# Optimization experiments

Measured on AMD Instinct MI355X. Metric: run time of the kernel, lower is better.

Reference implementation:

```python
import jax, jax.numpy as jnp
import numpy as np

B, T, C = 2, 1024, 1024
H = 16
D = C // H          # 64 head_dim
NHH = 4             # hyper n_heads
NL = 2              # hyper n_layers
RANK = 8
SCALE = 16.0 / RANK # alpha / rank


def _rope(x, cos, sin):
    # x: (B,H,T,D); cos/sin: (1,1,T,D//2)
    xe, xo = x[..., ::2], x[..., 1::2]
    return jnp.stack((xe * cos - xo * sin, xe * sin + xo * cos), axis=-1).reshape(x.shape)


def _mha(x, w_in, b_in, w_out, b_out, mask):
    # torch nn.MultiheadAttention (batch_first) with additive causal mask
    b, t, d = x.shape
    dh = d // NHH
    qkv = x @ w_in.T + b_in
    q, k, v = jnp.split(qkv, 3, axis=-1)
    split = lambda z: z.reshape(b, t, NHH, dh).transpose(0, 2, 1, 3)
    q, k, v = split(q), split(k), split(v)
    s = jnp.einsum('bhqd,bhkd->bhqk', q, k) / jnp.sqrt(jnp.float32(dh)) + mask
    o = jnp.einsum('bhqk,bhkd->bhqd', jax.nn.softmax(s, axis=-1), v)
    o = o.transpose(0, 2, 1, 3).reshape(b, t, d)
    return o @ w_out.T + b_out


def _tiny_head(x_h, in_w, in_b, out_w, out_b, a_w, b_w, mask):
    # x_h: (B,T,D); per-layer params stacked on axis 0 (NL)
    out = x_h
    for l in range(NL):
        out = _mha(out, in_w[l], in_b[l], out_w[l], out_b[l], mask)
    ctx = out.mean(axis=1)                       # (B,D)
    A = (ctx @ a_w.T).reshape(-1, D, RANK)       # (B,D,R)
    Bm = (ctx @ b_w.T).reshape(-1, RANK, D)      # (B,R,D)
    return A, Bm


def reference(x, cos, sin, c_attn_w, c_attn_b, c_proj_w, c_proj_b,
              hyper_in_w, hyper_in_b, hyper_out_w, hyper_out_b, toA_w, toB_w):
    mask = jnp.where(jnp.tril(jnp.ones((T, T), bool)), 0.0, -jnp.inf).astype(x.dtype)
    qkv = x @ c_attn_w.T + c_attn_b
    q, k, v = jnp.split(qkv, 3, axis=-1)
    split = lambda z: z.reshape(B, T, H, D).transpose(0, 2, 1, 3)  # (B,H,T,D)
    q, k, v = split(q), split(k), split(v)
    q = _rope(q, cos, sin)
    k = _rope(k, cos, sin)
    x_heads = split(x)
    # vmap over the 16 main heads; each gets its own TinyHeadTransformer params
    A, Bm = jax.vmap(_tiny_head, in_axes=(1, 0, 0, 0, 0, 0, 0, None))(
        x_heads, hyper_in_w, hyper_in_b, hyper_out_w, hyper_out_b, toA_w, toB_w, mask)
    # A: (H,B,D,R), Bm: (H,B,R,D)
    delta_v = jnp.einsum('bhti,hbir,hbro->bhto', v, A, Bm)
    v = v + SCALE * delta_v
    s = jnp.einsum('bhqd,bhkd->bhqk', q, k) / jnp.sqrt(jnp.float32(D)) + mask
    y = jnp.einsum('bhqk,bhkd->bhqd', jax.nn.softmax(s, axis=-1), v)
    y = y.transpose(0, 2, 1, 3).reshape(B, T, C)
    return y @ c_proj_w.T + c_proj_b


def setup_inputs() -> dict:
    key = jax.random.key(0)
    ks = jax.random.split(key, 8)
    inv_freq = 1.0 / (10000.0 ** (jnp.arange(0, D, 2, dtype=jnp.float32) / D))
    ang = jnp.arange(T, dtype=jnp.float32)[:, None] * inv_freq[None, :]
    cos = jnp.cos(ang)[None, None]  # (1,1,T,D/2)
    sin = jnp.sin(ang)[None, None]
    g = lambda k, shape, sc: jax.random.normal(k, shape, jnp.float32) * sc
    return dict(
        x=g(ks[0], (B, T, C), 1.0),
        cos=cos, sin=sin,
        c_attn_w=g(ks[1], (3 * C, C), 0.02),
        c_attn_b=jnp.zeros((3 * C,), jnp.float32),
        c_proj_w=g(ks[2], (C, C), 0.02),
        c_proj_b=jnp.zeros((C,), jnp.float32),
        hyper_in_w=g(ks[3], (H, NL, 3 * D, D), 0.02),
        hyper_in_b=jnp.zeros((H, NL, 3 * D), jnp.float32),
        hyper_out_w=g(ks[4], (H, NL, D, D), 0.02),
        hyper_out_b=jnp.zeros((H, NL, D), jnp.float32),
        toA_w=g(ks[5], (H, D * RANK, D), 0.02),
        toB_w=g(ks[6], (H, RANK * D, D), 0.02),
    )
```

## Files before the change

### kernel.cpp

```cpp
#include <hip/hip_runtime.h>

typedef unsigned short u16;
typedef short v8s __attribute__((ext_vector_type(8)));
typedef short v4s16 __attribute__((ext_vector_type(4)));
typedef float v4f __attribute__((ext_vector_type(4)));

#if defined(__has_builtin)
#  if __has_builtin(__builtin_amdgcn_exp2f)
#    define EXP2F(x) __builtin_amdgcn_exp2f(x)
#  else
#    define EXP2F(x) exp2f(x)
#  endif
#else
#  define EXP2F(x) exp2f(x)
#endif

__device__ __forceinline__ float bf2f(u16 u){
  union { float f; unsigned int i; } c; c.i = ((unsigned int)u) << 16; return c.f;
}
__device__ __forceinline__ u16 f2bf(float f){
  union { float f; unsigned int i; } c; c.f = f;
  unsigned int r = c.i + 0x7FFFu + ((c.i >> 16) & 1u);
  return (u16)(r >> 16);
}
__device__ __forceinline__ unsigned int cvt_pk_bf16(float lo, float hi){
  unsigned int r;
  asm("v_cvt_pk_bf16_f32 %0, %1, %2" : "=v"(r) : "v"(lo), "v"(hi));
  return r;
}

struct CvtArgs {
  const float* s[13];
  u16* d[13];
  int n[13];
  int bstart[14];
};
__global__ __launch_bounds__(256) void cvt_all(CvtArgs a) {
  int j = 0;
  #pragma unroll
  for (int i = 1; i < 13; i++) if ((int)blockIdx.x >= a.bstart[i]) j = i;
  const int lb = blockIdx.x - a.bstart[j];
  const long base = (long)lb * 1024 + threadIdx.x * 4;
  if (base < a.n[j]) {
    const float4 f = *(const float4*)&a.s[j][base];
    v4s16 o;
    o.x = (short)f2bf(f.x); o.y = (short)f2bf(f.y);
    o.z = (short)f2bf(f.z); o.w = (short)f2bf(f.w);
    *(v4s16*)&a.d[j][base] = o;
  }
}

template<int BM, int BN, bool OUTF>
__global__ __launch_bounds__(256) void gemm_nt(
    const u16* __restrict__ A, long aBatch, int lda,
    const u16* __restrict__ W, long wBatch,
    const u16* __restrict__ bias, long bBatch,
    void* __restrict__ Cp, long cBatch, int ldc,
    int K)
{
  constexpr int BK = 64, LDT = BK + 8;
  constexpr int AC = BM / 32;
  constexpr int BC = BN / 32;
  A    += (long)blockIdx.z * aBatch;
  W    += (long)blockIdx.z * wBatch;
  bias += (long)blockIdx.z * bBatch;
  const int row0 = blockIdx.y * BM, col0 = blockIdx.x * BN;
  __shared__ __align__(16) u16 As[BM * LDT];
  __shared__ __align__(16) u16 Bs[BN * LDT];
  const int tid = threadIdx.x, wid = tid >> 6, lane = tid & 63;
  constexpr int FM = (BM/2)/16, FN = (BN/2)/16;
  const int wr = (wid >> 1) * (BM/2), wc = (wid & 1) * (BN/2);
  v4f acc[FM][FN] = {};
  const int lr = lane & 15, lk = (lane >> 4) * 8;

  v8s areg[AC], breg[BC];
  auto loadAB = [&](int k0) {
    #pragma unroll
    for (int i = 0; i < AC; i++) {
      const int c = tid + i*256, r = c >> 3, cc = (c & 7) * 8;
      areg[i] = *(const v8s*)&A[(long)(row0 + r)*lda + k0 + cc];
    }
    #pragma unroll
    for (int i = 0; i < BC; i++) {
      const int c = tid + i*256, r = c >> 3, cc = (c & 7) * 8;
      breg[i] = *(const v8s*)&W[(long)(col0 + r)*K + k0 + cc];
    }
  };
  auto writeAB = [&]() {
    #pragma unroll
    for (int i = 0; i < AC; i++) {
      const int c = tid + i*256, r = c >> 3, cc = (c & 7) * 8;
      *(v8s*)&As[r*LDT + cc] = areg[i];
    }
    #pragma unroll
    for (int i = 0; i < BC; i++) {
      const int c = tid + i*256, r = c >> 3, cc = (c & 7) * 8;
      *(v8s*)&Bs[r*LDT + cc] = breg[i];
    }
  };

  loadAB(0); writeAB();
  __syncthreads();
  for (int k0 = 0; k0 < K; k0 += BK) {
    if (k0 + BK < K) loadAB(k0 + BK);
    #pragma unroll
    for (int ks = 0; ks < BK; ks += 32) {
      v8s af[FM], bfv[FN];
      #pragma unroll
      for (int i = 0; i < FM; i++) af[i]  = *(const v8s*)&As[(wr + i*16 + lr)*LDT + ks + lk];
      #pragma unroll
      for (int j = 0; j < FN; j++) bfv[j] = *(const v8s*)&Bs[(wc + j*16 + lr)*LDT + ks + lk];
      #pragma unroll
      for (int i = 0; i < FM; i++)
        #pragma unroll
        for (int j = 0; j < FN; j++)
          acc[i][j] = __builtin_amdgcn_mfma_f32_16x16x32_bf16(af[i], bfv[j], acc[i][j], 0, 0, 0);
    }
    __syncthreads();
    if (k0 + BK < K) {
      writeAB();
      __syncthreads();
    }
  }
  const int lc = lane & 15, lq = (lane >> 4) * 4;
  u16*   Cb = (u16*)Cp   + (long)blockIdx.z * cBatch;
  float* Cf = (float*)Cp + (long)blockIdx.z * cBatch;
  #pragma unroll
  for (int i = 0; i < FM; i++)
    #pragma unroll
    for (int j = 0; j < FN; j++) {
      const int cidx = col0 + wc + j*16 + lc;
      const float bv = bf2f(bias[cidx]);
      #pragma unroll
      for (int q = 0; q < 4; q++) {
        const int r = row0 + wr + i*16 + lq + q;
        if (OUTF) Cf[(long)r*ldc + cidx] = acc[i][j][q] + bv;
        else      Cb[(long)r*ldc + cidx] = f2bf(acc[i][j][q] + bv);
      }
    }
}

__global__ __launch_bounds__(256) void rope_split_k(
    const u16* __restrict__ qkv, const u16* __restrict__ cosb, const u16* __restrict__ sinb,
    u16* __restrict__ qr, u16* __restrict__ kr, u16* __restrict__ vv)
{
  const int idx  = blockIdx.x * 4 + (threadIdx.x >> 6);
  const int lane = threadIdx.x & 63;
  const int t = idx & 1023;
  const int h = (idx >> 10) & 15;
  const int b = idx >> 14;
  const u16* base = qkv + ((long)(b*1024 + t))*3072 + h*64;
  const int i = lane >> 1;
  const float c = bf2f(cosb[t*32 + i]), s = bf2f(sinb[t*32 + i]);
  const long ro = (long)idx * 64 + lane;
  float xe = bf2f(base[2*i]), xo = bf2f(base[2*i + 1]);
  qr[ro] = f2bf((lane & 1) ? xe*s + xo*c : xe*c - xo*s);
  xe = bf2f(base[1024 + 2*i]); xo = bf2f(base[1024 + 2*i + 1]);
  kr[ro] = f2bf((lane & 1) ? xe*s + xo*c : xe*c - xo*s);
  vv[ro] = base[2048 + lane];
}

template<int D>
__global__ __launch_bounds__(512) void flash_mfma(
    const u16* __restrict__ qb, const u16* __restrict__ kb,
    const u16* __restrict__ vb, u16* __restrict__ ob,
    float scale, int n1, int n2,
    long q0, long q1, long q2, int qs,
    long k0, long k1, long k2, int ks,
    long v0, long v1, long v2, int vs,
    long o0, long o1, long o2, int os)
{
  constexpr int KBLK = 64;
  constexpr int KD2 = (D < 32) ? 32 : D;
  constexpr int LDK = KD2 + 8;
  constexpr int LDV = KBLK + 8;
  constexpr int KD  = KD2 / 32;
  constexpr int NSUB = D / 16;
  constexpr int KCH = KBLK * (KD2/8);
  constexpr int VCH = (D/8) * KBLK;
  __shared__ __align__(16) u16 Ks[2][KBLK * LDK];
  __shared__ __align__(16) u16 Vs[2][D * LDV];

  const int tid = threadIdx.x, wid = tid >> 6, lane = tid & 63;
  const int lr = lane & 15, lg = lane >> 4;
  const int prob = blockIdx.x;
  const int p2 = prob % n2, p1 = (prob / n2) % n1, p0 = prob / (n2 * n1);
  const u16* qp = qb + p0*q0 + p1*q1 + p2*q2;
  const u16* kp = kb + p0*k0 + p1*k1 + p2*k2;
  const u16* vp = vb + p0*v0 + p1*v1 + p2*v2;
  u16* op = ob + p0*o0 + p1*o1 + p2*o2;

  const int ta = blockIdx.y;
  const int tb = 15 - ta;
  const int wtile = (wid & 4) ? tb : ta;
  const int wq = wtile * 64 + (wid & 3) * 16;
  const float scale2 = scale * 1.44269504f;

  v8s qf[KD];
  #pragma unroll
  for (int kd = 0; kd < KD; kd++) {
    const int dof = kd*32 + lg*8;
    v8s val = {};
    if (dof < D) val = *(const v8s*)&qp[(long)(wq + lr)*qs + dof];
    qf[kd] = val;
  }

  v4f Of[NSUB] = {};
  float m2 = -1.0e30f, l = 0.f;

  const int kkey = tid / (KD2/8), kd8 = (tid % (KD2/8)) * 8;
  const int vkey = tid / (D/8),  vd8 = (tid % (D/8)) * 8;
  v8s kreg = {}, vreg = {};

  if (tid < KCH) { v8s t = {}; if (kd8 < D) t = *(const v8s*)&kp[(long)kkey*ks + kd8]; kreg = t; }
  if (tid < VCH) vreg = *(const v8s*)&vp[(long)vkey*vs + vd8];
  if (tid < KCH) *(v8s*)&Ks[0][kkey*LDK + kd8] = kreg;
  if (tid < VCH) {
    #pragma unroll
    for (int j = 0; j < 8; j++) Vs[0][(vd8+j)*LDV + vkey] = vreg[j];
  }
  __syncthreads();

  for (int c = 0; c <= tb; c++) {
    const int cur = c & 1, nxt = cur ^ 1;
    if (c < tb) {
      const int kc2 = (c + 1) * 64;
      if (tid < KCH) { v8s t = {}; if (kd8 < D) t = *(const v8s*)&kp[(long)(kc2+kkey)*ks + kd8]; kreg = t; }
      if (tid < VCH) vreg = *(const v8s*)&vp[(long)(kc2+vkey)*vs + vd8];
    }
    if (c <= wtile) {
      const int kc = c * 64;
      v4f sf[4];
      #pragma unroll
      for (int f = 0; f < 4; f++) {
        v4f s = {};
        #pragma unroll
        for (int kd = 0; kd < KD; kd++) {
          const v8s kf = *(const v8s*)&Ks[cur][(f*16 + lr)*LDK + kd*32 + lg*8];
          s = __builtin_amdgcn_mfma_f32_16x16x32_bf16(kf, qf[kd], s, 0, 0, 0);
        }
        sf[f] = s;
      }
      const int qg = wq + lr;
      if (kc + 63 > wq) {
        #pragma unroll
        for (int f = 0; f < 4; f++)
          #pragma unroll
          for (int r = 0; r < 4; r++)
            sf[f][r] = (kc + 16*f + 4*lg + r <= qg) ? sf[f][r] : -3.0e38f;
      }
      float mx0 = fmaxf(fmaxf(sf[0][0], sf[0][1]), fmaxf(sf[0][2], sf[0][3]));
      float mx1 = fmaxf(fmaxf(sf[1][0], sf[1][1]), fmaxf(sf[1][2], sf[1][3]));
      float mx2 = fmaxf(fmaxf(sf[2][0], sf[2][1]), fmaxf(sf[2][2], sf[2][3]));
      float mx3 = fmaxf(fmaxf(sf[3][0], sf[3][1]), fmaxf(sf[3][2], sf[3][3]));
      float mx = fmaxf(fmaxf(mx0, mx1), fmaxf(mx2, mx3));
      mx = fmaxf(mx, __shfl_xor(mx, 16));
      mx = fmaxf(mx, __shfl_xor(mx, 32));
      const float mn2 = fmaxf(m2, mx * scale2);
      const float al = EXP2F(m2 - mn2);
      m2 = mn2;
      float pv[4][4];
      #pragma unroll
      for (int f = 0; f < 4; f++)
        #pragma unroll
        for (int r = 0; r < 4; r++)
          pv[f][r] = EXP2F(__builtin_fmaf(sf[f][r], scale2, -mn2));
      float s0 = (pv[0][0]+pv[0][1]) + (pv[0][2]+pv[0][3]);
      float s1 = (pv[1][0]+pv[1][1]) + (pv[1][2]+pv[1][3]);
      float s2 = (pv[2][0]+pv[2][1]) + (pv[2][2]+pv[2][3]);
      float s3 = (pv[3][0]+pv[3][1]) + (pv[3][2]+pv[3][3]);
      float ps = (s0+s1) + (s2+s3);
      ps += __shfl_xor(ps, 16);
      ps += __shfl_xor(ps, 32);
      l = l * al + ps;
      #pragma unroll
      for (int sub = 0; sub < NSUB; sub++)
        #pragma unroll
        for (int r = 0; r < 4; r++) Of[sub][r] *= al;
      unsigned int pw[8];
      #pragma unroll
      for (int f = 0; f < 4; f++) {
        pw[2*f]   = cvt_pk_bf16(pv[f][0], pv[f][1]);
        pw[2*f+1] = cvt_pk_bf16(pv[f][2], pv[f][3]);
      }
      #pragma unroll
      for (int kb2 = 0; kb2 < 2; kb2++) {
        union { unsigned int w[4]; v8s v; } pb;
        pb.w[0] = pw[4*kb2];   pb.w[1] = pw[4*kb2+1];
        pb.w[2] = pw[4*kb2+2]; pb.w[3] = pw[4*kb2+3];
        #pragma unroll
        for (int sub = 0; sub < NSUB; sub++) {
          union { v4s16 h[2]; v8s v; } va;
          const int vbase = (sub*16 + lr)*LDV + kb2*32 + 4*lg;
          va.h[0] = *(const v4s16*)&Vs[cur][vbase];
          va.h[1] = *(const v4s16*)&Vs[cur][vbase + 16];
          Of[sub] = __builtin_amdgcn_mfma_f32_16x16x32_bf16(va.v, pb.v, Of[sub], 0, 0, 0);
        }
      }
    }
    if (c < tb) {
      if (tid < KCH) *(v8s*)&Ks[nxt][kkey*LDK + kd8] = kreg;
      if (tid < VCH) {
        #pragma unroll
        for (int j = 0; j < 8; j++) Vs[nxt][(vd8+j)*LDV + vkey] = vreg[j];
      }
    }
    __syncthreads();
  }
  const float rl = __builtin_amdgcn_rcpf(l);
  #pragma unroll
  for (int sub = 0; sub < NSUB; sub++) {
    unsigned int w0 = cvt_pk_bf16(Of[sub][0]*rl, Of[sub][1]*rl);
    unsigned int w1 = cvt_pk_bf16(Of[sub][2]*rl, Of[sub][3]*rl);
    unsigned int* dst = (unsigned int*)&op[(long)(wq + lr)*os + sub*16 + 4*lg];
    dst[0] = w0; dst[1] = w1;
  }
}

__global__ __launch_bounds__(256) void ctx_mean_k(const u16* __restrict__ tb, float* __restrict__ ctx)
{
  const int hb = blockIdx.x;
  const int h = hb >> 1, b = hb & 1;
  const int d = threadIdx.x & 63, chunk = threadIdx.x >> 6;
  const u16* p = tb + (long)h*2048*64 + (long)b*1024*64 + d;
  float s = 0.f;
  for (int t = chunk*256; t < (chunk+1)*256; t++) s += bf2f(p[(long)t*64]);
  __shared__ float red[4][64];
  red[chunk][d] = s;
  __syncthreads();
  if (threadIdx.x < 64) {
    const float tot = red[0][d] + red[1][d] + red[2][d] + red[3][d];
    ctx[hb*64 + d] = tot * (1.0f/1024.0f);
  }
}

__global__ __launch_bounds__(256) void ab_proj_k(const float* __restrict__ ctx,
    const u16* __restrict__ toA, const u16* __restrict__ toB,
    float* __restrict__ Am, float* __restrict__ Bm)
{
  const int hb = blockIdx.x; const int h = hb >> 1;
  const float* c = ctx + hb * 64;
  for (int n = threadIdx.x; n < 512; n += 256) {
    const u16* wa = toA + ((long)h*512 + n) * 64;
    const u16* wb = toB + ((long)h*512 + n) * 64;
    float sa = 0.f, sb = 0.f;
    for (int i = 0; i < 64; i++) { sa += c[i]*bf2f(wa[i]); sb += c[i]*bf2f(wb[i]); }
    Am[hb*512 + n] = sa;
    Bm[hb*512 + n] = sb;
  }
}

__global__ __launch_bounds__(256) void delta_v_k(
    u16* __restrict__ v, const float* __restrict__ Am, const float* __restrict__ Bm)
{
  const long idx = (long)blockIdx.x * blockDim.x + threadIdx.x;
  const int h = (int)((idx >> 10) & 15);
  const int b = (int)(idx >> 14);
  u16* row = v + idx * 64;
  const float* A = Am + (h*2 + b) * 512;
  const float* B = Bm + (h*2 + b) * 512;
  float tmp[8] = {};
  #pragma unroll 8
  for (int d = 0; d < 64; d++) {
    const float vd = bf2f(row[d]);
    #pragma unroll
    for (int r = 0; r < 8; r++) tmp[r] += vd * A[d*8 + r];
  }
  #pragma unroll 8
  for (int d = 0; d < 64; d++) {
    float s = 0.f;
    #pragma unroll
    for (int r = 0; r < 8; r++) s += tmp[r] * B[r*64 + d];
    row[d] = f2bf(bf2f(row[d]) + 2.0f * s);
  }
}

extern "C" void kernel_launch(void* const* d_in, const int* in_sizes, int n_in,
                              void* d_out, int out_size, void* d_ws, size_t ws_size,
                              hipStream_t stream) {
  (void)in_sizes; (void)n_in; (void)out_size; (void)ws_size;
  float* out = (float*)d_out;

  char* ws = (char*)d_ws;
  size_t off = 0;
  auto alloc = [&](size_t bytes){ void* p = ws + off; off += (bytes + 255) & ~(size_t)255; return p; };

  static const int ns[13] = {2097152, 32768, 32768, 3145728, 3072, 1048576, 1024,
                             393216, 6144, 131072, 2048, 524288, 524288};
  u16* bufs[13];
  for (int i = 0; i < 13; i++) bufs[i] = (u16*)alloc((size_t)ns[i] * 2);
  u16* xb    = bufs[0];
  u16* cosb  = bufs[1];
  u16* sinb  = bufs[2];
  u16* attnw = bufs[3];
  u16* attnb = bufs[4];
  u16* projw = bufs[5];
  u16* projb = bufs[6];
  u16* hinw  = bufs[7];
  u16* hinb  = bufs[8];
  u16* houtw = bufs[9];
  u16* houtb = bufs[10];
  u16* toAb  = bufs[11];
  u16* toBb  = bufs[12];

  u16* qkv  = (u16*)alloc(6291456ull*2);
  u16* q_r  = (u16*)alloc(2097152ull*2);
  u16* k_r  = (u16*)alloc(2097152ull*2);
  u16* v    = (u16*)alloc(2097152ull*2);
  u16* tqkv = (u16*)alloc(6291456ull*2);
  u16* tatt = (u16*)alloc(2097152ull*2);
  u16* tb0  = (u16*)alloc(2097152ull*2);
  u16* tb1  = (u16*)alloc(2097152ull*2);
  u16* yat  = (u16*)alloc(2097152ull*2);
  float* ctx  = (float*)alloc(2048*4);
  float* Amat = (float*)alloc(16384*4);
  float* Bmat = (float*)alloc(16384*4);

  CvtArgs ca;
  int bacc = 0;
  for (int i = 0; i < 13; i++) {
    ca.s[i] = (const float*)d_in[i];
    ca.d[i] = bufs[i];
    ca.n[i] = ns[i];
    ca.bstart[i] = bacc;
    bacc += (ns[i] + 1023) / 1024;
  }
  ca.bstart[13] = bacc;
  cvt_all<<<dim3(bacc), 256, 0, stream>>>(ca);

  gemm_nt<64,128,false><<<dim3(24,32,1),256,0,stream>>>(xb,0,1024, attnw,0, attnb,0,
                                                        qkv,0,3072, 1024);
  rope_split_k<<<dim3(8192),256,0,stream>>>(qkv, cosb, sinb, q_r, k_r, v);

  const u16* tin = xb; long tinBatch = 64; int tinLda = 1024;
  u16* touts[2] = {tb0, tb1};
  for (int l = 0; l < 2; l++) {
    gemm_nt<64,64,false><<<dim3(3,32,16),256,0,stream>>>(tin, tinBatch, tinLda,
        hinw + (size_t)l*192*64, (long)2*192*64,
        hinb + (size_t)l*192,    (long)2*192,
        tqkv, (long)2048*192, 192, 64);
    flash_mfma<16><<<dim3(128,8),512,0,stream>>>(tqkv, tqkv+64, tqkv+128, tatt,
        0.25f, 2, 4,
        (long)2048*192, (long)1024*192, 16L, 192,
        (long)2048*192, (long)1024*192, 16L, 192,
        (long)2048*192, (long)1024*192, 16L, 192,
        (long)2048*64,  (long)1024*64,  16L, 64);
    gemm_nt<64,64,false><<<dim3(1,32,16),256,0,stream>>>(tatt, (long)2048*64, 64,
        houtw + (size_t)l*64*64, (long)2*64*64,
        houtb + (size_t)l*64,    (long)2*64,
        touts[l], (long)2048*64, 64, 64);
    tin = touts[l]; tinBatch = (long)2048*64; tinLda = 64;
  }
  ctx_mean_k<<<dim3(32),256,0,stream>>>(tb1, ctx);
  ab_proj_k<<<dim3(32),256,0,stream>>>(ctx, toAb, toBb, Amat, Bmat);
  delta_v_k<<<dim3(128),256,0,stream>>>(v, Amat, Bmat);

  flash_mfma<64><<<dim3(32,8),512,0,stream>>>(q_r, k_r, v, yat,
      0.125f, 16, 1,
      (long)16*1024*64, (long)1024*64, 0L, 64,
      (long)16*1024*64, (long)1024*64, 0L, 64,
      (long)16*1024*64, (long)1024*64, 0L, 64,
      (long)1024*1024,  64L,           0L, 1024);

  gemm_nt<64,64,true><<<dim3(16,32,1),256,0,stream>>>(yat,0,1024, projw,0, projb,0,
                                                      out,0,1024, 1024);
}
```

Before: 279.4 us.

## Fuse RoPE split into QKV GEMM, fuse ctx mean, widen flash key block

The QKV projection epilogue now applies RoPE and scatters straight into per-head q/k/v buffers, which removes the intermediate qkv tensor and the separate rope kernel. The last hyper out-projection GEMM reduces its columns and atomically adds the mean into ctx, with ctx zeroed by an extra block of the conversion kernel; this removes the ctx_mean kernel and the tb1 buffer. The flash kernel processes 128-key blocks instead of 64, which halves the loop iterations and barriers but raises register and LDS use. The QKV GEMM tile also drops from 64x128 to 64x64, and float atomics make the ctx sum order nondeterministic.

```diff
diff --git a/kernel.cpp b/kernel.cpp
--- a/kernel.cpp
+++ b/kernel.cpp
@@ -34,8 +34,15 @@
   u16* d[13];
   int n[13];
   int bstart[14];
+  float* ctxz;
 };
 __global__ __launch_bounds__(256) void cvt_all(CvtArgs a) {
+  if ((int)blockIdx.x >= a.bstart[13]) {
+    float4 z = {0.f, 0.f, 0.f, 0.f};
+    ((float4*)a.ctxz)[threadIdx.x] = z;
+    ((float4*)a.ctxz)[256 + threadIdx.x] = z;
+    return;
+  }
   int j = 0;
   #pragma unroll
   for (int i = 1; i < 13; i++) if ((int)blockIdx.x >= a.bstart[i]) j = i;
@@ -50,13 +57,16 @@
   }
 }
 
-template<int BM, int BN, bool OUTF>
+template<int BM, int BN, int EPI>
 __global__ __launch_bounds__(256) void gemm_nt(
     const u16* __restrict__ A, long aBatch, int lda,
     const u16* __restrict__ W, long wBatch,
     const u16* __restrict__ bias, long bBatch,
     void* __restrict__ Cp, long cBatch, int ldc,
-    int K)
+    int K,
+    const u16* __restrict__ cosb, const u16* __restrict__ sinb,
+    u16* __restrict__ q_r, u16* __restrict__ k_r, u16* __restrict__ v_out,
+    float* __restrict__ ctxp)
 {
   constexpr int BK = 64, LDT = BK + 8;
   constexpr int AC = BM / 32;
@@ -123,41 +133,69 @@
     }
   }
   const int lc = lane & 15, lq = (lane >> 4) * 4;
-  u16*   Cb = (u16*)Cp   + (long)blockIdx.z * cBatch;
-  float* Cf = (float*)Cp + (long)blockIdx.z * cBatch;
-  #pragma unroll
-  for (int i = 0; i < FM; i++)
+  if (EPI <= 1) {
+    u16*   Cb = (u16*)Cp   + (long)blockIdx.z * cBatch;
+    float* Cf = (float*)Cp + (long)blockIdx.z * cBatch;
+    #pragma unroll
+    for (int i = 0; i < FM; i++)
+      #pragma unroll
+      for (int j = 0; j < FN; j++) {
+        const int cidx = col0 + wc + j*16 + lc;
+        const float bv = bf2f(bias[cidx]);
+        #pragma unroll
+        for (int q = 0; q < 4; q++) {
+          const int r = row0 + wr + i*16 + lq + q;
+          if (EPI == 1) Cf[(long)r*ldc + cidx] = acc[i][j][q] + bv;
+          else          Cb[(long)r*ldc + cidx] = f2bf(acc[i][j][q] + bv);
+        }
+      }
+  } else if (EPI == 2) {
+    #pragma unroll
+    for (int i = 0; i < FM; i++)
+      #pragma unroll
+      for (int j = 0; j < FN; j++) {
+        const int cidx = col0 + wc + j*16 + lc;
+        const float bv = bf2f(bias[cidx]);
+        const int which = cidx >> 10;
+        const int h = (cidx & 1023) >> 6;
+        const int d = cidx & 63;
+        u16* dst = (which == 0) ? q_r : (which == 1) ? k_r : v_out;
+        #pragma unroll
+        for (int q = 0; q < 4; q++) {
+          const int r = row0 + wr + i*16 + lq + q;
+          const int b = r >> 10, t = r & 1023;
+          float val = acc[i][j][q] + bv;
+          float par = __shfl_xor(val, 1);
+          float outv;
+          if (which == 2) {
+            outv = val;
+          } else {
+            const int i2 = d >> 1;
+            const float cc = bf2f(cosb[(t << 5) + i2]);
+            const float ss = bf2f(sinb[(t << 5) + i2]);
+            outv = (d & 1) ? __builtin_fmaf(par, ss,  val*cc)
+                           : __builtin_fmaf(val, cc, -par*ss);
+          }
+          dst[((long)((b << 4) + h)*1024 + t)*64 + d] = f2bf(outv);
+        }
+      }
+  } else {
+    const float inv = 1.0f/1024.0f;
+    const int hb = (blockIdx.z << 1) + (row0 >> 10);
     #pragma unroll
     for (int j = 0; j < FN; j++) {
       const int cidx = col0 + wc + j*16 + lc;
       const float bv = bf2f(bias[cidx]);
-      #pragma unroll
-      for (int q = 0; q < 4; q++) {
-        const int r = row0 + wr + i*16 + lq + q;
-        if (OUTF) Cf[(long)r*ldc + cidx] = acc[i][j][q] + bv;
-        else      Cb[(long)r*ldc + cidx] = f2bf(acc[i][j][q] + bv);
-      }
-    }
-}
-
-__global__ __launch_bounds__(256) void rope_split_k(
-    const u16* __restrict__ qkv, const u16* __restrict__ cosb, const u16* __restrict__ sinb,
-    u16* __restrict__ qr, u16* __restrict__ kr, u16* __restrict__ vv)
-{
-  const int idx  = blockIdx.x * 4 + (threadIdx.x >> 6);
-  const int lane = threadIdx.x & 63;
-  const int t = idx & 1023;
-  const int h = (idx >> 10) & 15;
-  const int b = idx >> 14;
-  const u16* base = qkv + ((long)(b*1024 + t))*3072 + h*64;
-  const int i = lane >> 1;
-  const float c = bf2f(cosb[t*32 + i]), s = bf2f(sinb[t*32 + i]);
-  const long ro = (long)idx * 64 + lane;
-  float xe = bf2f(base[2*i]), xo = bf2f(base[2*i + 1]);
-  qr[ro] = f2bf((lane & 1) ? xe*s + xo*c : xe*c - xo*s);
-  xe = bf2f(base[1024 + 2*i]); xo = bf2f(base[1024 + 2*i + 1]);
-  kr[ro] = f2bf((lane & 1) ? xe*s + xo*c : xe*c - xo*s);
-  vv[ro] = base[2048 + lane];
+      float p = (float)(FM*4) * bv;
+      #pragma unroll
+      for (int i = 0; i < FM; i++)
+        #pragma unroll
+        for (int q = 0; q < 4; q++) p += acc[i][j][q];
+      p += __shfl_xor(p, 16);
+      p += __shfl_xor(p, 32);
+      if (lane < 16) atomicAdd(&ctxp[hb*64 + cidx], p * inv);
+    }
+  }
 }
 
 template<int D>
@@ -170,7 +208,9 @@
     long v0, long v1, long v2, int vs,
     long o0, long o1, long o2, int os)
 {
-  constexpr int KBLK = 64;
+  constexpr int KBLK = 128;
+  constexpr int NF  = KBLK / 16;
+  constexpr int NKB = KBLK / 32;
   constexpr int KD2 = (D < 32) ? 32 : D;
   constexpr int LDK = KD2 + 8;
   constexpr int LDV = KBLK + 8;
@@ -178,6 +218,8 @@
   constexpr int NSUB = D / 16;
   constexpr int KCH = KBLK * (KD2/8);
   constexpr int VCH = (D/8) * KBLK;
+  constexpr int KIT = (KCH + 511) / 512;
+  constexpr int VIT = (VCH + 511) / 512;
   __shared__ __align__(16) u16 Ks[2][KBLK * LDK];
   __shared__ __align__(16) u16 Vs[2][D * LDV];
 
@@ -191,9 +233,10 @@
   u16* op = ob + p0*o0 + p1*o1 + p2*o2;
 
   const int ta = blockIdx.y;
-  const int tb = 15 - ta;
-  const int wtile = (wid & 4) ? tb : ta;
+  const int tbt = 15 - ta;
+  const int wtile = (wid & 4) ? tbt : ta;
   const int wq = wtile * 64 + (wid & 3) * 16;
+  const int nchb = (tbt >> 1) + 1;
   const float scale2 = scale * 1.44269504f;
 
   v8s qf[KD];
@@ -208,31 +251,60 @@
   v4f Of[NSUB] = {};
   float m2 = -1.0e30f, l = 0.f;
 
-  const int kkey = tid / (KD2/8), kd8 = (tid % (KD2/8)) * 8;
-  const int vkey = tid / (D/8),  vd8 = (tid % (D/8)) * 8;
-  v8s kreg = {}, vreg = {};
-
-  if (tid < KCH) { v8s t = {}; if (kd8 < D) t = *(const v8s*)&kp[(long)kkey*ks + kd8]; kreg = t; }
-  if (tid < VCH) vreg = *(const v8s*)&vp[(long)vkey*vs + vd8];
-  if (tid < KCH) *(v8s*)&Ks[0][kkey*LDK + kd8] = kreg;
-  if (tid < VCH) {
-    #pragma unroll
-    for (int j = 0; j < 8; j++) Vs[0][(vd8+j)*LDV + vkey] = vreg[j];
-  }
+  v8s kreg[KIT], vreg[VIT];
+  auto loadK = [&](int kc) {
+    #pragma unroll
+    for (int i = 0; i < KIT; i++) {
+      const int idx = tid + i*512;
+      if (idx < KCH) {
+        const int key = idx / (KD2/8), d8 = (idx % (KD2/8)) * 8;
+        v8s t = {};
+        if (d8 < D) t = *(const v8s*)&kp[(long)(kc + key)*ks + d8];
+        kreg[i] = t;
+      }
+    }
+  };
+  auto loadV = [&](int kc) {
+    #pragma unroll
+    for (int i = 0; i < VIT; i++) {
+      const int idx = tid + i*512;
+      if (idx < VCH) {
+        const int key = idx / (D/8), d8 = (idx % (D/8)) * 8;
+        vreg[i] = *(const v8s*)&vp[(long)(kc + key)*vs + d8];
+      }
+    }
+  };
+  auto writeKV = [&](int buf) {
+    #pragma unroll
+    for (int i = 0; i < KIT; i++) {
+      const int idx = tid + i*512;
+      if (idx < KCH) {
+        const int key = idx / (KD2/8), d8 = (idx % (KD2/8)) * 8;
+        *(v8s*)&Ks[buf][key*LDK + d8] = kreg[i];
+      }
+    }
+    #pragma unroll
+    for (int i = 0; i < VIT; i++) {
+      const int idx = tid + i*512;
+      if (idx < VCH) {
+        const int key = idx / (D/8), d8 = (idx % (D/8)) * 8;
+        #pragma unroll
+        for (int j = 0; j < 8; j++) Vs[buf][(d8+j)*LDV + key] = vreg[i][j];
+      }
+    }
+  };
+
+  loadK(0); loadV(0); writeKV(0);
   __syncthreads();
 
-  for (int c = 0; c <= tb; c++) {
+  for (int c = 0; c < nchb; c++) {
     const int cur = c & 1, nxt = cur ^ 1;
-    if (c < tb) {
-      const int kc2 = (c + 1) * 64;
-      if (tid < KCH) { v8s t = {}; if (kd8 < D) t = *(const v8s*)&kp[(long)(kc2+kkey)*ks + kd8]; kreg = t; }
-      if (tid < VCH) vreg = *(const v8s*)&vp[(long)(kc2+vkey)*vs + vd8];
-    }
-    if (c <= wtile) {
-      const int kc = c * 64;
-      v4f sf[4];
-      #pragma unroll
-      for (int f = 0; f < 4; f++) {
+    if (c + 1 < nchb) { loadK((c+1)*KBLK); loadV((c+1)*KBLK); }
+    const int kc = c * KBLK;
+    if (kc <= wq + 15) {
+      v4f sf[NF];
+      #pragma unroll
+      for (int f = 0; f < NF; f++) {
         v4f s = {};
         #pragma unroll
         for (int kd = 0; kd < KD; kd++) {
@@ -242,34 +314,31 @@
         sf[f] = s;
       }
       const int qg = wq + lr;
-      if (kc + 63 > wq) {
-        #pragma unroll
-        for (int f = 0; f < 4; f++)
+      if (kc + KBLK - 1 > wq) {
+        #pragma unroll
+        for (int f = 0; f < NF; f++)
           #pragma unroll
           for (int r = 0; r < 4; r++)
             sf[f][r] = (kc + 16*f + 4*lg + r <= qg) ? sf[f][r] : -3.0e38f;
       }
-      float mx0 = fmaxf(fmaxf(sf[0][0], sf[0][1]), fmaxf(sf[0][2], sf[0][3]));
-      float mx1 = fmaxf(fmaxf(sf[1][0], sf[1][1]), fmaxf(sf[1][2], sf[1][3]));
-      float mx2 = fmaxf(fmaxf(sf[2][0], sf[2][1]), fmaxf(sf[2][2], sf[2][3]));
-      float mx3 = fmaxf(fmaxf(sf[3][0], sf[3][1]), fmaxf(sf[3][2], sf[3][3]));
-      float mx = fmaxf(fmaxf(mx0, mx1), fmaxf(mx2, mx3));
+      float mx = -3.0e38f;
+      #pragma unroll
+      for (int f = 0; f < NF; f++)
+        mx = fmaxf(mx, fmaxf(fmaxf(sf[f][0], sf[f][1]), fmaxf(sf[f][2], sf[f][3])));
       mx = fmaxf(mx, __shfl_xor(mx, 16));
       mx = fmaxf(mx, __shfl_xor(mx, 32));
       const float mn2 = fmaxf(m2, mx * scale2);
       const float al = EXP2F(m2 - mn2);
       m2 = mn2;
-      float pv[4][4];
-      #pragma unroll
-      for (int f = 0; f < 4; f++)
+      float pv[NF][4];
+      float ps = 0.f;
+      #pragma unroll
+      for (int f = 0; f < NF; f++) {
         #pragma unroll
         for (int r = 0; r < 4; r++)
           pv[f][r] = EXP2F(__builtin_fmaf(sf[f][r], scale2, -mn2));
-      float s0 = (pv[0][0]+pv[0][1]) + (pv[0][2]+pv[0][3]);
-      float s1 = (pv[1][0]+pv[1][1]) + (pv[1][2]+pv[1][3]);
-      float s2 = (pv[2][0]+pv[2][1]) + (pv[2][2]+pv[2][3]);
-      float s3 = (pv[3][0]+pv[3][1]) + (pv[3][2]+pv[3][3]);
-      float ps = (s0+s1) + (s2+s3);
+        ps += (pv[f][0] + pv[f][1]) + (pv[f][2] + pv[f][3]);
+      }
       ps += __shfl_xor(ps, 16);
       ps += __shfl_xor(ps, 32);
       l = l * al + ps;
@@ -277,14 +346,14 @@
       for (int sub = 0; sub < NSUB; sub++)
         #pragma unroll
         for (int r = 0; r < 4; r++) Of[sub][r] *= al;
-      unsigned int pw[8];
-      #pragma unroll
-      for (int f = 0; f < 4; f++) {
+      unsigned int pw[2*NF];
+      #pragma unroll
+      for (int f = 0; f < NF; f++) {
         pw[2*f]   = cvt_pk_bf16(pv[f][0], pv[f][1]);
         pw[2*f+1] = cvt_pk_bf16(pv[f][2], pv[f][3]);
       }
       #pragma unroll
-      for (int kb2 = 0; kb2 < 2; kb2++) {
+      for (int kb2 = 0; kb2 < NKB; kb2++) {
         union { unsigned int w[4]; v8s v; } pb;
         pb.w[0] = pw[4*kb2];   pb.w[1] = pw[4*kb2+1];
         pb.w[2] = pw[4*kb2+2]; pb.w[3] = pw[4*kb2+3];
@@ -298,13 +367,7 @@
         }
       }
     }
-    if (c < tb) {
-      if (tid < KCH) *(v8s*)&Ks[nxt][kkey*LDK + kd8] = kreg;
-      if (tid < VCH) {
-        #pragma unroll
-        for (int j = 0; j < 8; j++) Vs[nxt][(vd8+j)*LDV + vkey] = vreg[j];
-      }
-    }
+    if (c + 1 < nchb) writeKV(nxt);
     __syncthreads();
   }
   const float rl = __builtin_amdgcn_rcpf(l);
@@ -314,23 +377,6 @@
     unsigned int w1 = cvt_pk_bf16(Of[sub][2]*rl, Of[sub][3]*rl);
     unsigned int* dst = (unsigned int*)&op[(long)(wq + lr)*os + sub*16 + 4*lg];
     dst[0] = w0; dst[1] = w1;
-  }
-}
-
-__global__ __launch_bounds__(256) void ctx_mean_k(const u16* __restrict__ tb, float* __restrict__ ctx)
-{
-  const int hb = blockIdx.x;
-  const int h = hb >> 1, b = hb & 1;
-  const int d = threadIdx.x & 63, chunk = threadIdx.x >> 6;
-  const u16* p = tb + (long)h*2048*64 + (long)b*1024*64 + d;
-  float s = 0.f;
-  for (int t = chunk*256; t < (chunk+1)*256; t++) s += bf2f(p[(long)t*64]);
-  __shared__ float red[4][64];
-  red[chunk][d] = s;
-  __syncthreads();
-  if (threadIdx.x < 64) {
-    const float tot = red[0][d] + red[1][d] + red[2][d] + red[3][d];
-    ctx[hb*64 + d] = tot * (1.0f/1024.0f);
   }
 }
 
@@ -403,14 +449,12 @@
   u16* toAb  = bufs[11];
   u16* toBb  = bufs[12];
 
-  u16* qkv  = (u16*)alloc(6291456ull*2);
   u16* q_r  = (u16*)alloc(2097152ull*2);
   u16* k_r  = (u16*)alloc(2097152ull*2);
   u16* v    = (u16*)alloc(2097152ull*2);
   u16* tqkv = (u16*)alloc(6291456ull*2);
   u16* tatt = (u16*)alloc(2097152ull*2);
   u16* tb0  = (u16*)alloc(2097152ull*2);
-  u16* tb1  = (u16*)alloc(2097152ull*2);
   u16* yat  = (u16*)alloc(2097152ull*2);
   float* ctx  = (float*)alloc(2048*4);
   float* Amat = (float*)alloc(16384*4);
@@ -426,32 +470,41 @@
     bacc += (ns[i] + 1023) / 1024;
   }
   ca.bstart[13] = bacc;
-  cvt_all<<<dim3(bacc), 256, 0, stream>>>(ca);
-
-  gemm_nt<64,128,false><<<dim3(24,32,1),256,0,stream>>>(xb,0,1024, attnw,0, attnb,0,
-                                                        qkv,0,3072, 1024);
-  rope_split_k<<<dim3(8192),256,0,stream>>>(qkv, cosb, sinb, q_r, k_r, v);
-
-  const u16* tin = xb; long tinBatch = 64; int tinLda = 1024;
-  u16* touts[2] = {tb0, tb1};
-  for (int l = 0; l < 2; l++) {
-    gemm_nt<64,64,false><<<dim3(3,32,16),256,0,stream>>>(tin, tinBatch, tinLda,
-        hinw + (size_t)l*192*64, (long)2*192*64,
-        hinb + (size_t)l*192,    (long)2*192,
-        tqkv, (long)2048*192, 192, 64);
-    flash_mfma<16><<<dim3(128,8),512,0,stream>>>(tqkv, tqkv+64, tqkv+128, tatt,
-        0.25f, 2, 4,
-        (long)2048*192, (long)1024*192, 16L, 192,
-        (long)2048*192, (long)1024*192, 16L, 192,
-        (long)2048*192, (long)1024*192, 16L, 192,
-        (long)2048*64,  (long)1024*64,  16L, 64);
-    gemm_nt<64,64,false><<<dim3(1,32,16),256,0,stream>>>(tatt, (long)2048*64, 64,
-        houtw + (size_t)l*64*64, (long)2*64*64,
-        houtb + (size_t)l*64,    (long)2*64,
-        touts[l], (long)2048*64, 64, 64);
-    tin = touts[l]; tinBatch = (long)2048*64; tinLda = 64;
-  }
-  ctx_mean_k<<<dim3(32),256,0,stream>>>(tb1, ctx);
+  ca.ctxz = ctx;
+  cvt_all<<<dim3(bacc + 1), 256, 0, stream>>>(ca);
+
+  gemm_nt<64,64,2><<<dim3(48,32,1),256,0,stream>>>(xb,0,1024, attnw,0, attnb,0,
+      nullptr,0,0, 1024, cosb, sinb, q_r, k_r, v, nullptr);
+
+  gemm_nt<64,64,0><<<dim3(3,32,16),256,0,stream>>>(xb, 64L, 1024,
+      hinw, (long)2*192*64, hinb, (long)2*192,
+      tqkv, (long)2048*192, 192, 64,
+      nullptr, nullptr, nullptr, nullptr, nullptr, nullptr);
+  flash_mfma<16><<<dim3(128,8),512,0,stream>>>(tqkv, tqkv+64, tqkv+128, tatt,
+      0.25f, 2, 4,
+      (long)2048*192, (long)1024*192, 16L, 192,
+      (long)2048*192, (long)1024*192, 16L, 192,
+      (long)2048*192, (long)1024*192, 16L, 192,
+      (long)2048*64,  (long)1024*64,  16L, 64);
+  gemm_nt<64,64,0><<<dim3(1,32,16),256,0,stream>>>(tatt, (long)2048*64, 64,
+      houtw, (long)2*64*64, houtb, (long)2*64,
+      tb0, (long)2048*64, 64, 64,
+      nullptr, nullptr, nullptr, nullptr, nullptr, nullptr);
+  gemm_nt<64,64,0><<<dim3(3,32,16),256,0,stream>>>(tb0, (long)2048*64, 64,
+      hinw + (size_t)192*64, (long)2*192*64, hinb + 192, (long)2*192,
+      tqkv, (long)2048*192, 192, 64,
+      nullptr, nullptr, nullptr, nullptr, nullptr, nullptr);
+  flash_mfma<16><<<dim3(128,8),512,0,stream>>>(tqkv, tqkv+64, tqkv+128, tatt,
+      0.25f, 2, 4,
+      (long)2048*192, (long)1024*192, 16L, 192,
+      (long)2048*192, (long)1024*192, 16L, 192,
+      (long)2048*192, (long)1024*192, 16L, 192,
+      (long)2048*64,  (long)1024*64,  16L, 64);
+  gemm_nt<64,64,3><<<dim3(1,32,16),256,0,stream>>>(tatt, (long)2048*64, 64,
+      houtw + (size_t)64*64, (long)2*64*64, houtb + 64, (long)2*64,
+      nullptr, 0, 0, 64,
+      nullptr, nullptr, nullptr, nullptr, nullptr, ctx);
+
   ab_proj_k<<<dim3(32),256,0,stream>>>(ctx, toAb, toBb, Amat, Bmat);
   delta_v_k<<<dim3(128),256,0,stream>>>(v, Amat, Bmat);
 
@@ -462,6 +515,7 @@
       (long)16*1024*64, (long)1024*64, 0L, 64,
       (long)1024*1024,  64L,           0L, 1024);
 
-  gemm_nt<64,64,true><<<dim3(16,32,1),256,0,stream>>>(yat,0,1024, projw,0, projb,0,
-                                                      out,0,1024, 1024);
-}
+  gemm_nt<64,64,1><<<dim3(16,32,1),256,0,stream>>>(yat,0,1024, projw,0, projb,0,
+      out,0,1024, 1024,
+      nullptr, nullptr, nullptr, nullptr, nullptr, nullptr);
+}
```

After: 274.8 us. About the same (-1.6%).
